# Kernel tuning notes

Hardware: AMD Instinct MI355X
Metric: run time of the kernel (lower is better)

## Reference

```python
import jax, jax.numpy as jnp
import numpy as np

B, C, H, W = 64, 3, 384, 384


def setup_inputs() -> dict:
    key = jax.random.key(0)
    k1, k2 = jax.random.split(key)
    imgs = jax.random.normal(k1, (B, C, H, W), dtype=jnp.float32)
    eye = jnp.broadcast_to(jnp.eye(2, 3, dtype=jnp.float32), (B, 2, 3))
    theta = eye + 0.05 * jax.random.normal(k2, (B, 2, 3), dtype=jnp.float32)
    return {"imgs": imgs, "theta": theta}


def _gen_affine_grid(theta, h, w):
    # Mirrors torchvision functional_tensor._gen_affine_grid (align_corners=False style).
    # theta: [2,3]; returns normalized grid [h, w, 2] in [-1, 1].
    d = 0.5
    xs = jnp.linspace(-w * 0.5 + d, w * 0.5 + d - 1, w, dtype=jnp.float32)  # [w]
    ys = jnp.linspace(-h * 0.5 + d, h * 0.5 + d - 1, h, dtype=jnp.float32)  # [h]
    # base_grid[y, x] = (xs[x], ys[y], 1)
    xg, yg = jnp.meshgrid(xs, ys)  # each [h, w]
    ones = jnp.ones_like(xg)
    base = jnp.stack([xg, yg, ones], axis=-1)  # [h, w, 3]
    scale = jnp.array([0.5 * w, 0.5 * h], dtype=jnp.float32)
    rescaled_theta = theta.T / scale  # [3, 2]
    return base @ rescaled_theta  # [h, w, 2]


def _grid_sample_bilinear(img, grid):
    # img: [C, H, W], grid: [H, W, 2] normalized coords, zeros padding,
    # align_corners=False (torch grid_sample semantics).
    c, h, w = img.shape
    ix = (grid[..., 0] + 1.0) * w * 0.5 - 0.5  # [H, W]
    iy = (grid[..., 1] + 1.0) * h * 0.5 - 0.5
    x0 = jnp.floor(ix)
    y0 = jnp.floor(iy)
    wx1 = ix - x0
    wy1 = iy - y0
    wx0 = 1.0 - wx1
    wy0 = 1.0 - wy1

    def gather(xi, yi):
        valid = (xi >= 0) & (xi < w) & (yi >= 0) & (yi < h)
        xc = jnp.clip(xi, 0, w - 1).astype(jnp.int32)
        yc = jnp.clip(yi, 0, h - 1).astype(jnp.int32)
        v = img[:, yc, xc]  # [C, H, W] gather
        return v * valid.astype(img.dtype)

    out = (gather(x0, y0) * (wx0 * wy0)
           + gather(x0 + 1, y0) * (wx1 * wy0)
           + gather(x0, y0 + 1) * (wx0 * wy1)
           + gather(x0 + 1, y0 + 1) * (wx1 * wy1))
    return out  # [C, H, W]


def reference(imgs, theta):
    b, c, h, w = imgs.shape

    def per_image(img, th):
        grid = _gen_affine_grid(th, h, w)
        return _grid_sample_bilinear(img, grid)

    return jax.vmap(per_image)(imgs, theta)  # [B, C, H, W]
```

## Files before the change

### kernel.cpp

```cpp
#include <hip/hip_runtime.h>

#define B_ 64
#define C_ 3
#define H_ 384
#define W_ 384
#define HW_ (H_ * W_)

__global__ __launch_bounds__(256) void affine_sample_kernel(
    const float* __restrict__ imgs,
    const float* __restrict__ theta,
    float* __restrict__ out)
{
    int idx = blockIdx.x * 256 + threadIdx.x;
    int x = idx % W_;
    int t = idx / W_;
    int y = t % H_;
    int b = t / H_;

    const float* th = theta + b * 6;
    float t00 = th[0], t01 = th[1], t02 = th[2];
    float t10 = th[3], t11 = th[4], t12 = th[5];

    float xg = (float)x - 191.5f;
    float yg = (float)y - 191.5f;

    float ix = fmaf(xg, t00, fmaf(yg, t01, t02)) + 191.5f;
    float iy = fmaf(xg, t10, fmaf(yg, t11, t12)) + 191.5f;

    float x0f = floorf(ix);
    float y0f = floorf(iy);
    float wx1 = ix - x0f;
    float wy1 = iy - y0f;
    float wx0 = 1.0f - wx1;
    float wy0 = 1.0f - wy1;

    float x1f = x0f + 1.0f;
    float y1f = y0f + 1.0f;

    bool vx0 = (x0f >= 0.0f) && (x0f < (float)W_);
    bool vx1 = (x1f >= 0.0f) && (x1f < (float)W_);
    bool vy0 = (y0f >= 0.0f) && (y0f < (float)H_);
    bool vy1 = (y1f >= 0.0f) && (y1f < (float)H_);

    int x0 = (int)fminf(fmaxf(x0f, 0.0f), (float)(W_ - 1));
    int x1 = (int)fminf(fmaxf(x1f, 0.0f), (float)(W_ - 1));
    int y0 = (int)fminf(fmaxf(y0f, 0.0f), (float)(H_ - 1));
    int y1 = (int)fminf(fmaxf(y1f, 0.0f), (float)(H_ - 1));

    float w00 = wx0 * wy0 * ((vx0 && vy0) ? 1.0f : 0.0f);
    float w01 = wx1 * wy0 * ((vx1 && vy0) ? 1.0f : 0.0f);
    float w10 = wx0 * wy1 * ((vx0 && vy1) ? 1.0f : 0.0f);
    float w11 = wx1 * wy1 * ((vx1 && vy1) ? 1.0f : 0.0f);

    int o00 = y0 * W_ + x0;
    int o01 = y0 * W_ + x1;
    int o10 = y1 * W_ + x0;
    int o11 = y1 * W_ + x1;

    const float* bimg = imgs + (size_t)b * (C_ * HW_);
    float* bout = out + (size_t)b * (C_ * HW_) + y * W_ + x;

#pragma unroll
    for (int c = 0; c < C_; ++c) {
        const float* p = bimg + c * HW_;
        float v00 = p[o00];
        float v01 = p[o01];
        float v10 = p[o10];
        float v11 = p[o11];
        float r = fmaf(v00, w00, fmaf(v01, w01, fmaf(v10, w10, v11 * w11)));
        bout[c * HW_] = r;
    }
}

extern "C" void kernel_launch(void* const* d_in, const int* in_sizes, int n_in,
                              void* d_out, int out_size, void* d_ws, size_t ws_size,
                              hipStream_t stream) {
    const float* imgs = (const float*)d_in[0];
    const float* theta = (const float*)d_in[1];
    float* out = (float*)d_out;
    int total = B_ * H_ * W_;
    affine_sample_kernel<<<total / 256, 256, 0, stream>>>(imgs, theta, out);
}
```

Before: 227.1 us.

## Process two pixels per thread, vectorize stores, remap blocks across XCDs

Each thread now computes two adjacent output pixels and writes them with float2 stores, halving the thread count and sharing the row-dependent affine terms. Block indices are permuted so that consecutive spatial chunks map to the same XCD (8-way interleave), with the aim of improving L2 locality for the gather reads. The batch index is made wave-uniform via readfirstlane so theta loads become scalar. This raises register use per thread, and the remap assumes the grid size divides evenly by 8.

Result: slower. 252.3 us (+11.1%).

```diff
diff --git a/kernel.cpp b/kernel.cpp
--- a/kernel.cpp
+++ b/kernel.cpp
@@ -11,64 +11,89 @@
     const float* __restrict__ theta,
     float* __restrict__ out)
 {
-    int idx = blockIdx.x * 256 + threadIdx.x;
-    int x = idx % W_;
-    int t = idx / W_;
+    int nb = gridDim.x;
+    int chunk = nb >> 3;
+    int bid = blockIdx.x;
+    int sb = (bid & 7) * chunk + (bid >> 3);
+
+    int idx = sb * 256 + threadIdx.x;
+    int px = idx * 2;
+    int x = px % W_;
+    int t = px / W_;
     int y = t % H_;
     int b = t / H_;
+    b = __builtin_amdgcn_readfirstlane(b);
 
     const float* th = theta + b * 6;
     float t00 = th[0], t01 = th[1], t02 = th[2];
     float t10 = th[3], t11 = th[4], t12 = th[5];
 
-    float xg = (float)x - 191.5f;
     float yg = (float)y - 191.5f;
-
-    float ix = fmaf(xg, t00, fmaf(yg, t01, t02)) + 191.5f;
-    float iy = fmaf(xg, t10, fmaf(yg, t11, t12)) + 191.5f;
-
-    float x0f = floorf(ix);
-    float y0f = floorf(iy);
-    float wx1 = ix - x0f;
-    float wy1 = iy - y0f;
-    float wx0 = 1.0f - wx1;
-    float wy0 = 1.0f - wy1;
-
-    float x1f = x0f + 1.0f;
-    float y1f = y0f + 1.0f;
-
-    bool vx0 = (x0f >= 0.0f) && (x0f < (float)W_);
-    bool vx1 = (x1f >= 0.0f) && (x1f < (float)W_);
-    bool vy0 = (y0f >= 0.0f) && (y0f < (float)H_);
-    bool vy1 = (y1f >= 0.0f) && (y1f < (float)H_);
-
-    int x0 = (int)fminf(fmaxf(x0f, 0.0f), (float)(W_ - 1));
-    int x1 = (int)fminf(fmaxf(x1f, 0.0f), (float)(W_ - 1));
-    int y0 = (int)fminf(fmaxf(y0f, 0.0f), (float)(H_ - 1));
-    int y1 = (int)fminf(fmaxf(y1f, 0.0f), (float)(H_ - 1));
-
-    float w00 = wx0 * wy0 * ((vx0 && vy0) ? 1.0f : 0.0f);
-    float w01 = wx1 * wy0 * ((vx1 && vy0) ? 1.0f : 0.0f);
-    float w10 = wx0 * wy1 * ((vx0 && vy1) ? 1.0f : 0.0f);
-    float w11 = wx1 * wy1 * ((vx1 && vy1) ? 1.0f : 0.0f);
-
-    int o00 = y0 * W_ + x0;
-    int o01 = y0 * W_ + x1;
-    int o10 = y1 * W_ + x0;
-    int o11 = y1 * W_ + x1;
+    float iy_base = fmaf(yg, t01, t02) + 191.5f;
+    float ix_base_y = fmaf(yg, t11, t12) + 191.5f;
 
     const float* bimg = imgs + (size_t)b * (C_ * HW_);
     float* bout = out + (size_t)b * (C_ * HW_) + y * W_ + x;
 
+    float res[2][C_];
+    int offs[2][4];
+    float wts[2][4];
+
+#pragma unroll
+    for (int j = 0; j < 2; ++j) {
+        float xg = (float)(x + j) - 191.5f;
+        float ix = fmaf(xg, t00, iy_base);
+        float iy = fmaf(xg, t10, ix_base_y);
+
+        float x0f = floorf(ix);
+        float y0f = floorf(iy);
+        float wx1 = ix - x0f;
+        float wy1 = iy - y0f;
+        float wx0 = 1.0f - wx1;
+        float wy0 = 1.0f - wy1;
+        float x1f = x0f + 1.0f;
+        float y1f = y0f + 1.0f;
+
+        bool vx0 = (x0f >= 0.0f) && (x0f < (float)W_);
+        bool vx1 = (x1f >= 0.0f) && (x1f < (float)W_);
+        bool vy0 = (y0f >= 0.0f) && (y0f < (float)H_);
+        bool vy1 = (y1f >= 0.0f) && (y1f < (float)H_);
+
+        int x0 = (int)fminf(fmaxf(x0f, 0.0f), (float)(W_ - 1));
+        int x1 = (int)fminf(fmaxf(x1f, 0.0f), (float)(W_ - 1));
+        int y0 = (int)fminf(fmaxf(y0f, 0.0f), (float)(H_ - 1));
+        int y1 = (int)fminf(fmaxf(y1f, 0.0f), (float)(H_ - 1));
+
+        wts[j][0] = wx0 * wy0 * ((vx0 && vy0) ? 1.0f : 0.0f);
+        wts[j][1] = wx1 * wy0 * ((vx1 && vy0) ? 1.0f : 0.0f);
+        wts[j][2] = wx0 * wy1 * ((vx0 && vy1) ? 1.0f : 0.0f);
+        wts[j][3] = wx1 * wy1 * ((vx1 && vy1) ? 1.0f : 0.0f);
+
+        offs[j][0] = y0 * W_ + x0;
+        offs[j][1] = y0 * W_ + x1;
+        offs[j][2] = y1 * W_ + x0;
+        offs[j][3] = y1 * W_ + x1;
+    }
+
 #pragma unroll
     for (int c = 0; c < C_; ++c) {
         const float* p = bimg + c * HW_;
-        float v00 = p[o00];
-        float v01 = p[o01];
-        float v10 = p[o10];
-        float v11 = p[o11];
-        float r = fmaf(v00, w00, fmaf(v01, w01, fmaf(v10, w10, v11 * w11)));
-        bout[c * HW_] = r;
+#pragma unroll
+        for (int j = 0; j < 2; ++j) {
+            float v00 = p[offs[j][0]];
+            float v01 = p[offs[j][1]];
+            float v10 = p[offs[j][2]];
+            float v11 = p[offs[j][3]];
+            res[j][c] = fmaf(v00, wts[j][0],
+                        fmaf(v01, wts[j][1],
+                        fmaf(v10, wts[j][2], v11 * wts[j][3])));
+        }
+    }
+
+#pragma unroll
+    for (int c = 0; c < C_; ++c) {
+        float2 r = make_float2(res[0][c], res[1][c]);
+        *(float2*)(bout + c * HW_) = r;
     }
 }
 
@@ -78,6 +103,7 @@
     const float* imgs = (const float*)d_in[0];
     const float* theta = (const float*)d_in[1];
     float* out = (float*)d_out;
-    int total = B_ * H_ * W_;
-    affine_sample_kernel<<<total / 256, 256, 0, stream>>>(imgs, theta, out);
+    int total_threads = B_ * H_ * W_ / 2;
+    int blocks = total_threads / 256;
+    affine_sample_kernel<<<blocks, 256, 0, stream>>>(imgs, theta, out);
 }
```

## Stage affine source footprint per 32x32 output tile in LDS

Applied to the files above, without the earlier changes.

Each block now handles a 32x32 output tile. It computes the bounding box of the source region that the affine map touches, loads that region for all three channels into shared memory with zero padding, and does the bilinear gathers from LDS. If the footprint is larger than 48x48 it falls back to direct global gathers. The goal is to replace scattered global gathers with coalesced row loads and LDS reuse, at the cost of a sync, about 28KB of LDS per block, and a branch.

New measurement: 266.3 us. 17.3% more time.

```diff
diff --git a/kernel.cpp b/kernel.cpp
--- a/kernel.cpp
+++ b/kernel.cpp
@@ -6,69 +6,168 @@
 #define W_ 384
 #define HW_ (H_ * W_)
 
-__global__ __launch_bounds__(256) void affine_sample_kernel(
+#define TW 32
+#define TH 32
+#define TILES_X (W_ / TW)
+#define TILES_Y (H_ / TH)
+#define SRCW 48
+#define SRCH 48
+#define SRCP 49
+
+__global__ __launch_bounds__(256) void affine_tile_kernel(
     const float* __restrict__ imgs,
     const float* __restrict__ theta,
     float* __restrict__ out)
 {
-    int idx = blockIdx.x * 256 + threadIdx.x;
-    int x = idx % W_;
-    int t = idx / W_;
-    int y = t % H_;
-    int b = t / H_;
+    __shared__ float lds[C_ * SRCH * SRCP];
+
+    int bid = blockIdx.x;
+    int b = bid / (TILES_X * TILES_Y);
+    int r = bid % (TILES_X * TILES_Y);
+    int tileY = (r / TILES_X) * TH;
+    int tileX = (r % TILES_X) * TW;
 
     const float* th = theta + b * 6;
     float t00 = th[0], t01 = th[1], t02 = th[2];
     float t10 = th[3], t11 = th[4], t12 = th[5];
 
-    float xg = (float)x - 191.5f;
-    float yg = (float)y - 191.5f;
+    int tx = threadIdx.x & 31;
+    int ty = threadIdx.x >> 5;
 
-    float ix = fmaf(xg, t00, fmaf(yg, t01, t02)) + 191.5f;
-    float iy = fmaf(xg, t10, fmaf(yg, t11, t12)) + 191.5f;
+    float xg0 = (float)tileX - 191.5f;
+    float xg1 = (float)(tileX + TW - 1) - 191.5f;
+    float yg0 = (float)tileY - 191.5f;
+    float yg1 = (float)(tileY + TH - 1) - 191.5f;
 
-    float x0f = floorf(ix);
-    float y0f = floorf(iy);
-    float wx1 = ix - x0f;
-    float wy1 = iy - y0f;
-    float wx0 = 1.0f - wx1;
-    float wy0 = 1.0f - wy1;
+    float i0 = fmaf(yg0, t01, t02);
+    float i1 = fmaf(yg1, t01, t02);
+    float ixa = fmaf(xg0, t00, i0) + 191.5f;
+    float ixb = fmaf(xg1, t00, i0) + 191.5f;
+    float ixc = fmaf(xg0, t00, i1) + 191.5f;
+    float ixd = fmaf(xg1, t00, i1) + 191.5f;
+    float ixmin = fminf(fminf(ixa, ixb), fminf(ixc, ixd));
+    float ixmax = fmaxf(fmaxf(ixa, ixb), fmaxf(ixc, ixd));
 
-    float x1f = x0f + 1.0f;
-    float y1f = y0f + 1.0f;
+    float j0 = fmaf(yg0, t11, t12);
+    float j1 = fmaf(yg1, t11, t12);
+    float iya = fmaf(xg0, t10, j0) + 191.5f;
+    float iyb = fmaf(xg1, t10, j0) + 191.5f;
+    float iyc = fmaf(xg0, t10, j1) + 191.5f;
+    float iyd = fmaf(xg1, t10, j1) + 191.5f;
+    float iymin = fminf(fminf(iya, iyb), fminf(iyc, iyd));
+    float iymax = fmaxf(fmaxf(iya, iyb), fmaxf(iyc, iyd));
 
-    bool vx0 = (x0f >= 0.0f) && (x0f < (float)W_);
-    bool vx1 = (x1f >= 0.0f) && (x1f < (float)W_);
-    bool vy0 = (y0f >= 0.0f) && (y0f < (float)H_);
-    bool vy1 = (y1f >= 0.0f) && (y1f < (float)H_);
-
-    int x0 = (int)fminf(fmaxf(x0f, 0.0f), (float)(W_ - 1));
-    int x1 = (int)fminf(fmaxf(x1f, 0.0f), (float)(W_ - 1));
-    int y0 = (int)fminf(fmaxf(y0f, 0.0f), (float)(H_ - 1));
-    int y1 = (int)fminf(fmaxf(y1f, 0.0f), (float)(H_ - 1));
-
-    float w00 = wx0 * wy0 * ((vx0 && vy0) ? 1.0f : 0.0f);
-    float w01 = wx1 * wy0 * ((vx1 && vy0) ? 1.0f : 0.0f);
-    float w10 = wx0 * wy1 * ((vx0 && vy1) ? 1.0f : 0.0f);
-    float w11 = wx1 * wy1 * ((vx1 && vy1) ? 1.0f : 0.0f);
-
-    int o00 = y0 * W_ + x0;
-    int o01 = y0 * W_ + x1;
-    int o10 = y1 * W_ + x0;
-    int o11 = y1 * W_ + x1;
+    int srcX0 = (int)floorf(ixmin);
+    int srcX1 = (int)floorf(ixmax) + 1;
+    int srcY0 = (int)floorf(iymin);
+    int srcY1 = (int)floorf(iymax) + 1;
+    int srcW = srcX1 - srcX0 + 1;
+    int srcH = srcY1 - srcY0 + 1;
 
     const float* bimg = imgs + (size_t)b * (C_ * HW_);
-    float* bout = out + (size_t)b * (C_ * HW_) + y * W_ + x;
+    float* bout = out + (size_t)b * (C_ * HW_);
+
+    if (srcW <= SRCW && srcH <= SRCH) {
+        for (int c = 0; c < C_; ++c) {
+            const float* p = bimg + c * HW_;
+            float* l = lds + c * (SRCH * SRCP);
+            for (int sy = ty; sy < srcH; sy += 8) {
+                int gy = srcY0 + sy;
+                bool vy = (gy >= 0) & (gy < H_);
+                int gyc = min(max(gy, 0), H_ - 1);
+                const float* row = p + gyc * W_;
+                for (int sx = tx; sx < srcW; sx += 32) {
+                    int gx = srcX0 + sx;
+                    bool v = vy & (gx >= 0) & (gx < W_);
+                    int gxc = min(max(gx, 0), W_ - 1);
+                    float val = row[gxc];
+                    l[sy * SRCP + sx] = v ? val : 0.0f;
+                }
+            }
+        }
+        __syncthreads();
 
 #pragma unroll
-    for (int c = 0; c < C_; ++c) {
-        const float* p = bimg + c * HW_;
-        float v00 = p[o00];
-        float v01 = p[o01];
-        float v10 = p[o10];
-        float v11 = p[o11];
-        float r = fmaf(v00, w00, fmaf(v01, w01, fmaf(v10, w10, v11 * w11)));
-        bout[c * HW_] = r;
+        for (int k = 0; k < 4; ++k) {
+            int oy = tileY + ty + k * 8;
+            int ox = tileX + tx;
+            float xg = (float)ox - 191.5f;
+            float yg = (float)oy - 191.5f;
+            float ix = fmaf(xg, t00, fmaf(yg, t01, t02)) + 191.5f;
+            float iy = fmaf(xg, t10, fmaf(yg, t11, t12)) + 191.5f;
+
+            float x0f = floorf(ix);
+            float y0f = floorf(iy);
+            float wx1 = ix - x0f;
+            float wy1 = iy - y0f;
+            float wx0 = 1.0f - wx1;
+            float wy0 = 1.0f - wy1;
+            float w00 = wx0 * wy0, w01 = wx1 * wy0;
+            float w10 = wx0 * wy1, w11 = wx1 * wy1;
+
+            int lx = (int)x0f - srcX0;
+            int ly = (int)y0f - srcY0;
+            int base = ly * SRCP + lx;
+
+#pragma unroll
+            for (int c = 0; c < C_; ++c) {
+                const float* l = lds + c * (SRCH * SRCP) + base;
+                float v00 = l[0];
+                float v01 = l[1];
+                float v10 = l[SRCP];
+                float v11 = l[SRCP + 1];
+                float res = fmaf(v00, w00, fmaf(v01, w01,
+                            fmaf(v10, w10, v11 * w11)));
+                bout[c * HW_ + oy * W_ + ox] = res;
+            }
+        }
+    } else {
+#pragma unroll
+        for (int k = 0; k < 4; ++k) {
+            int oy = tileY + ty + k * 8;
+            int ox = tileX + tx;
+            float xg = (float)ox - 191.5f;
+            float yg = (float)oy - 191.5f;
+            float ix = fmaf(xg, t00, fmaf(yg, t01, t02)) + 191.5f;
+            float iy = fmaf(xg, t10, fmaf(yg, t11, t12)) + 191.5f;
+
+            float x0f = floorf(ix);
+            float y0f = floorf(iy);
+            float wx1 = ix - x0f;
+            float wy1 = iy - y0f;
+            float wx0 = 1.0f - wx1;
+            float wy0 = 1.0f - wy1;
+            float x1f = x0f + 1.0f;
+            float y1f = y0f + 1.0f;
+
+            bool vx0 = (x0f >= 0.0f) && (x0f < (float)W_);
+            bool vx1 = (x1f >= 0.0f) && (x1f < (float)W_);
+            bool vy0 = (y0f >= 0.0f) && (y0f < (float)H_);
+            bool vy1 = (y1f >= 0.0f) && (y1f < (float)H_);
+
+            int x0 = (int)fminf(fmaxf(x0f, 0.0f), (float)(W_ - 1));
+            int x1 = (int)fminf(fmaxf(x1f, 0.0f), (float)(W_ - 1));
+            int y0 = (int)fminf(fmaxf(y0f, 0.0f), (float)(H_ - 1));
+            int y1 = (int)fminf(fmaxf(y1f, 0.0f), (float)(H_ - 1));
+
+            float w00 = wx0 * wy0 * ((vx0 && vy0) ? 1.0f : 0.0f);
+            float w01 = wx1 * wy0 * ((vx1 && vy0) ? 1.0f : 0.0f);
+            float w10 = wx0 * wy1 * ((vx0 && vy1) ? 1.0f : 0.0f);
+            float w11 = wx1 * wy1 * ((vx1 && vy1) ? 1.0f : 0.0f);
+
+            int o00 = y0 * W_ + x0;
+            int o01 = y0 * W_ + x1;
+            int o10 = y1 * W_ + x0;
+            int o11 = y1 * W_ + x1;
+
+#pragma unroll
+            for (int c = 0; c < C_; ++c) {
+                const float* p = bimg + c * HW_;
+                float res = fmaf(p[o00], w00, fmaf(p[o01], w01,
+                            fmaf(p[o10], w10, p[o11] * w11)));
+                bout[c * HW_ + oy * W_ + ox] = res;
+            }
+        }
     }
 }
 
@@ -78,6 +177,6 @@
     const float* imgs = (const float*)d_in[0];
     const float* theta = (const float*)d_in[1];
     float* out = (float*)d_out;
-    int total = B_ * H_ * W_;
-    affine_sample_kernel<<<total / 256, 256, 0, stream>>>(imgs, theta, out);
+    int blocks = B_ * TILES_X * TILES_Y;
+    affine_tile_kernel<<<blocks, 256, 0, stream>>>(imgs, theta, out);
 }
```
